# Kernel optimization log

Measured on AMD Instinct MI355X. Metric: run time of the kernel, lower is better.

## Reference

```python
import jax, jax.numpy as jnp
import numpy as np

B, S, D, H = 4, 1024, 1024, 16
HD = D // H  # head dim = 64


def setup_inputs() -> dict:
    key = jax.random.key(0)
    ks = jax.random.split(key, 12)
    inv = 1.0 / np.sqrt(D)
    inp = {
        "q": jax.random.normal(ks[0], (B, S, D), jnp.float32),
        "k": jax.random.normal(ks[1], (B, S, D), jnp.float32),
        "v": jax.random.normal(ks[2], (B, S, D), jnp.float32),
        # additive-style mask: 1 where attention is disallowed (causal)
        "mask": jnp.triu(jnp.ones((S, S), jnp.float32), k=1)[None, None, :, :],
        "Wq": jax.random.normal(ks[3], (D, D), jnp.float32) * inv,
        "bq": jnp.zeros((D,), jnp.float32),
        "Wk": jax.random.normal(ks[4], (D, D), jnp.float32) * inv,
        "bk": jnp.zeros((D,), jnp.float32),
        "Wv": jax.random.normal(ks[5], (D, D), jnp.float32) * inv,
        "bv": jnp.zeros((D,), jnp.float32),
        "Wo": jax.random.normal(ks[6], (D, D), jnp.float32) * inv,
        "bo": jnp.zeros((D,), jnp.float32),
    }
    return inp


def _split_heads(x):
    # [b, s, (h d)] -> [b, h, s, d]
    b, s, _ = x.shape
    return x.reshape(b, s, H, HD).transpose(0, 2, 1, 3)


def reference(q, k, v, mask, Wq, bq, Wk, bk, Wv, bv, Wo, bo):
    query = _split_heads(q @ Wq + bq)   # [b,h,s,d]
    key = _split_heads(k @ Wk + bk)
    value = _split_heads(v @ Wv + bv)

    scores = jnp.einsum("bhqd,bhkd->bhqk", query, key) / np.sqrt(HD)
    scores = scores + mask * (-1e12)
    attention_weights = jax.nn.softmax(scores, axis=-1)  # [b,h,s,s]
    attn = jnp.einsum("bhqk,bhkd->bhqd", attention_weights, value)

    # dropout is identity in eval mode
    attn = attn.transpose(0, 2, 1, 3).reshape(q.shape[0], q.shape[1], D)
    out = attn @ Wo + bo
    return out, attention_weights
```

## Files before the change

### kernel.cpp

```cpp
#include <hip/hip_runtime.h>
#include <hip/hip_bf16.h>

#define B_ 4
#define S_ 1024
#define D_ 1024
#define H_ 16
#define HD_ 64
#define M_ (B_*S_)
#define NT_ (S_/64)

typedef __attribute__((ext_vector_type(8))) short bf16x8;
typedef __attribute__((ext_vector_type(8))) unsigned short u16x8;
typedef __attribute__((ext_vector_type(4))) float f32x4;

typedef __attribute__((address_space(1))) const unsigned int g_uint;
typedef __attribute__((address_space(3))) unsigned int l_uint;

__device__ __forceinline__ unsigned short f2bf(float f) {
  unsigned int x = __builtin_bit_cast(unsigned int, f);
  unsigned int r = (x + 0x7fffu + ((x >> 16) & 1u)) >> 16;
  return (unsigned short)r;
}
__device__ __forceinline__ float bf2f(unsigned short u) {
  unsigned int x = ((unsigned int)u) << 16;
  return __builtin_bit_cast(float, x);
}
__device__ __forceinline__ void load_lds16(const ushort* g, ushort* l) {
  __builtin_amdgcn_global_load_lds((g_uint*)g, (l_uint*)l, 16, 0, 0);
}

__global__ void cvt3(const float* __restrict__ q, const float* __restrict__ k,
                     const float* __restrict__ v, ushort* __restrict__ qo,
                     ushort* __restrict__ ko, ushort* __restrict__ vo) {
  const float* s; ushort* d;
  switch (blockIdx.y) {
    case 0: s = q; d = qo; break;
    case 1: s = k; d = ko; break;
    default: s = v; d = vo; break;
  }
  int n4 = (M_ * D_) / 4;
  for (int i = blockIdx.x * blockDim.x + threadIdx.x; i < n4; i += gridDim.x * blockDim.x) {
    float4 x = reinterpret_cast<const float4*>(s)[i];
    ushort4 o;
    o.x = f2bf(x.x); o.y = f2bf(x.y); o.z = f2bf(x.z); o.w = f2bf(x.w);
    reinterpret_cast<ushort4*>(d)[i] = o;
  }
}

__global__ void tr4(const float* __restrict__ Wq, const float* __restrict__ Wk,
                    const float* __restrict__ Wv, const float* __restrict__ Wo,
                    ushort* __restrict__ q, ushort* __restrict__ k,
                    ushort* __restrict__ v, ushort* __restrict__ o) {
  const float* W; ushort* WT;
  switch (blockIdx.z) {
    case 0: W = Wq; WT = q; break;
    case 1: W = Wk; WT = k; break;
    case 2: W = Wv; WT = v; break;
    default: W = Wo; WT = o; break;
  }
  __shared__ float tile[32][33];
  int tx = threadIdx.x & 31, ty = threadIdx.x >> 5;
  int bx = blockIdx.x * 32, by = blockIdx.y * 32;
  for (int r = 0; r < 32; r += 8)
    tile[ty + r][tx] = W[(size_t)(by + ty + r) * D_ + bx + tx];
  __syncthreads();
  for (int r = 0; r < 32; r += 8)
    WT[(size_t)(bx + ty + r) * D_ + by + tx] = f2bf(tile[tx][ty + r]);
}

template <int BF16OUT>
__device__ __forceinline__ void gemm_body(const ushort* __restrict__ A,
                                          const ushort* __restrict__ Bt,
                                          const float* __restrict__ bias,
                                          void* __restrict__ Cp,
                                          int bm, int bn, int N, int K) {
  __shared__ ushort Al[128 * 64];
  __shared__ ushort Bl[128 * 64];
  const int tid = threadIdx.x;
  const int wave = tid >> 6, lane = tid & 63;
  const int r0 = lane & 15, kq = lane >> 4;
  const int wr = wave >> 1, wc = wave & 1;
  const int sl = lane >> 3;
  const int sc8 = ((lane & 7) ^ sl) * 8;
  f32x4 zero = {0.f, 0.f, 0.f, 0.f};
  f32x4 acc[4][4];
#pragma unroll
  for (int m = 0; m < 4; ++m)
#pragma unroll
    for (int n = 0; n < 4; ++n) acc[m][n] = zero;

  for (int kt = 0; kt < K; kt += 64) {
    __syncthreads();
#pragma unroll
    for (int i = 0; i < 4; ++i) {
      int c = wave * 4 + i;
      load_lds16(A  + (size_t)(bm + c * 8 + sl) * K + kt + sc8, &Al[c * 512]);
      load_lds16(Bt + (size_t)(bn + c * 8 + sl) * K + kt + sc8, &Bl[c * 512]);
    }
    __syncthreads();
#pragma unroll
    for (int kk = 0; kk < 2; ++kk) {
      bf16x8 a[4], b[4];
#pragma unroll
      for (int m = 0; m < 4; ++m)
        a[m] = *(const bf16x8*)&Al[(wr * 64 + m * 16 + r0) * 64 + (((kk * 4 + kq) ^ (r0 & 7)) * 8)];
#pragma unroll
      for (int n = 0; n < 4; ++n)
        b[n] = *(const bf16x8*)&Bl[(wc * 64 + n * 16 + r0) * 64 + (((kk * 4 + kq) ^ (r0 & 7)) * 8)];
#pragma unroll
      for (int m = 0; m < 4; ++m)
#pragma unroll
        for (int n = 0; n < 4; ++n)
          acc[m][n] = __builtin_amdgcn_mfma_f32_16x16x32_bf16(a[m], b[n], acc[m][n], 0, 0, 0);
    }
  }

#pragma unroll
  for (int m = 0; m < 4; ++m) {
#pragma unroll
    for (int n = 0; n < 4; ++n) {
      int col = bn + wc * 64 + n * 16 + r0;
      float bv = bias[col];
#pragma unroll
      for (int j = 0; j < 4; ++j) {
        int row = bm + wr * 64 + m * 16 + kq * 4 + j;
        float v = acc[m][n][j] + bv;
        if (BF16OUT) ((ushort*)Cp)[(size_t)row * N + col] = f2bf(v);
        else         ((float*)Cp)[(size_t)row * N + col] = v;
      }
    }
  }
}

__global__ __launch_bounds__(256) void gemm_qkv(const ushort* __restrict__ qa,
                                                const ushort* __restrict__ ka,
                                                const ushort* __restrict__ va,
                                                const ushort* __restrict__ WqT,
                                                const ushort* __restrict__ WkT,
                                                const ushort* __restrict__ WvT,
                                                const float* __restrict__ bq,
                                                const float* __restrict__ bk,
                                                const float* __restrict__ bv,
                                                ushort* __restrict__ Qo,
                                                ushort* __restrict__ Ko,
                                                ushort* __restrict__ Vo) {
  const ushort* A; const ushort* Bt; const float* bias; ushort* C;
  switch (blockIdx.z) {
    case 0: A = qa; Bt = WqT; bias = bq; C = Qo; break;
    case 1: A = ka; Bt = WkT; bias = bk; C = Ko; break;
    default: A = va; Bt = WvT; bias = bv; C = Vo; break;
  }
  gemm_body<1>(A, Bt, bias, C, blockIdx.x * 128, blockIdx.y * 128, D_, D_);
}

__global__ __launch_bounds__(256) void gemm_out(const ushort* __restrict__ A,
                                                const ushort* __restrict__ Bt,
                                                const float* __restrict__ bias,
                                                float* __restrict__ C) {
  gemm_body<0>(A, Bt, bias, C, blockIdx.x * 128, blockIdx.y * 128, D_, D_);
}

__global__ __launch_bounds__(256) void attn_fused(const ushort* __restrict__ Qb,
                                                  const ushort* __restrict__ Kb,
                                                  const ushort* __restrict__ Vb,
                                                  float* __restrict__ wout,
                                                  ushort* __restrict__ ctx) {
  const int id = blockIdx.x;
  const int h = (id & 7) | (((id >> 3) & 1) << 3);
  const int b = (id >> 4) & 3;
  const int px = id >> 6;
  const int tid = threadIdx.x, wave = tid >> 6, lane = tid & 63;
  const int r0 = lane & 15, kq = lane >> 4;
  const int sl = lane >> 3;
  const int sc8 = ((lane & 7) ^ sl) * 8;
  __shared__ ushort Kt[2][64 * 64];
  __shared__ ushort Vt[2][64 * 64];
  __shared__ ushort Wl[4][16 * 64];
  __shared__ float rs_lds[4][16];
  float* wbase = wout + (size_t)((b * H_ + h) * S_) * S_;
  const size_t bh_off = ((size_t)(b * S_)) * D_ + (size_t)h * 64;

  for (int pp = 0; pp < 2; ++pp) {
    const int qt = pp ? (NT_ - 1 - px) : px;
    __syncthreads();

    const ushort* Qg = Qb + bh_off + (size_t)(qt * 64 + wave * 16 + r0) * D_ + kq * 8;
    bf16x8 qa0 = *(const bf16x8*)Qg;
    bf16x8 qa1 = *(const bf16x8*)(Qg + 32);
    const int grow0 = qt * 64 + wave * 16 + kq * 4;

    auto stage_K = [&](int buf, int vb) {
      const ushort* Kg = Kb + bh_off + (size_t)(vb * 64) * D_;
#pragma unroll
      for (int i = 0; i < 2; ++i) {
        int c = wave * 2 + i;
        load_lds16(Kg + (size_t)(c * 8 + sl) * D_ + sc8, &Kt[buf][c * 512]);
      }
    };

    int cur = 0;
    stage_K(0, 0);
    float partial[4] = {0.f, 0.f, 0.f, 0.f};
    for (int vb = 0; vb <= qt; ++vb) {
      asm volatile("s_waitcnt vmcnt(0)" ::: "memory");
      __builtin_amdgcn_s_barrier();
      if (vb < qt) stage_K(cur ^ 1, vb + 1);
      const bool diag = (vb == qt);
#pragma unroll
      for (int jt = 0; jt < 4; ++jt) {
        int krow = jt * 16 + r0;
        bf16x8 kb0 = *(const bf16x8*)&Kt[cur][krow * 64 + ((kq ^ (r0 & 7)) * 8)];
        bf16x8 kb1 = *(const bf16x8*)&Kt[cur][krow * 64 + (((4 + kq) ^ (r0 & 7)) * 8)];
        f32x4 sc = {0.f, 0.f, 0.f, 0.f};
        sc = __builtin_amdgcn_mfma_f32_16x16x32_bf16(qa0, kb0, sc, 0, 0, 0);
        sc = __builtin_amdgcn_mfma_f32_16x16x32_bf16(qa1, kb1, sc, 0, 0, 0);
        int col = vb * 64 + krow;
#pragma unroll
        for (int j = 0; j < 4; ++j) {
          float e = (diag && col > grow0 + j) ? 0.f : __expf(sc[j] * 0.125f);
          partial[j] += e;
        }
      }
      cur ^= 1;
    }
    float rs[4];
#pragma unroll
    for (int j = 0; j < 4; ++j) {
      float s = partial[j];
#pragma unroll
      for (int off = 1; off < 16; off <<= 1) s += __shfl_xor(s, off, 64);
      rs[j] = 1.f / s;
    }
    if (r0 == 0) {
#pragma unroll
      for (int j = 0; j < 4; ++j) rs_lds[wave][kq * 4 + j] = rs[j];
    }

    f32x4 zero = {0.f, 0.f, 0.f, 0.f};
    f32x4 cacc[4];
#pragma unroll
    for (int nt = 0; nt < 4; ++nt) cacc[nt] = zero;

    __syncthreads();
    uint4 vr[2];
    auto vload = [&](int vb) {
      const ushort* Vg = Vb + bh_off + (size_t)(vb * 64) * D_;
      vr[0] = *(const uint4*)&Vg[(size_t)lane * D_ + (size_t)(wave * 2 + 0) * 8];
      vr[1] = *(const uint4*)&Vg[(size_t)lane * D_ + (size_t)(wave * 2 + 1) * 8];
    };
    auto vwrite = [&](int buf) {
#pragma unroll
      for (int it = 0; it < 2; ++it) {
        int seg = wave * 2 + it;
        ushort tmp[8];
        *(uint4*)tmp = vr[it];
#pragma unroll
        for (int e = 0; e < 8; ++e) Vt[buf][(seg * 8 + e) * 64 + (lane ^ (e << 3))] = tmp[e];
      }
    };
    cur = 0;
    stage_K(0, 0);
    vload(0);
    vwrite(0);
    for (int vb = 0; vb <= qt; ++vb) {
      asm volatile("s_waitcnt vmcnt(0) lgkmcnt(0)" ::: "memory");
      __builtin_amdgcn_s_barrier();
      if (vb < qt) { stage_K(cur ^ 1, vb + 1); vload(vb + 1); }
      const bool diag = (vb == qt);
#pragma unroll
      for (int jt = 0; jt < 4; ++jt) {
        int krow = jt * 16 + r0;
        bf16x8 kb0 = *(const bf16x8*)&Kt[cur][krow * 64 + ((kq ^ (r0 & 7)) * 8)];
        bf16x8 kb1 = *(const bf16x8*)&Kt[cur][krow * 64 + (((4 + kq) ^ (r0 & 7)) * 8)];
        f32x4 sc = {0.f, 0.f, 0.f, 0.f};
        sc = __builtin_amdgcn_mfma_f32_16x16x32_bf16(qa0, kb0, sc, 0, 0, 0);
        sc = __builtin_amdgcn_mfma_f32_16x16x32_bf16(qa1, kb1, sc, 0, 0, 0);
        int col = vb * 64 + krow;
#pragma unroll
        for (int j = 0; j < 4; ++j) {
          int rowW = kq * 4 + j;
          float e = (diag && col > grow0 + j) ? 0.f : __expf(sc[j] * 0.125f);
          Wl[wave][rowW * 64 + ((jt * 16 + r0) ^ ((rowW & 7) << 3))] = f2bf(e);
        }
      }
#pragma unroll
      for (int ks = 0; ks < 2; ++ks) {
        bf16x8 af = *(const bf16x8*)&Wl[wave][r0 * 64 + (((ks * 4 + kq) ^ (r0 & 7)) * 8)];
#pragma unroll
        for (int nt = 0; nt < 4; ++nt) {
          bf16x8 vf = *(const bf16x8*)&Vt[cur][(nt * 16 + r0) * 64 + (((ks * 4 + kq) ^ (r0 & 7)) * 8)];
          cacc[nt] = __builtin_amdgcn_mfma_f32_16x16x32_bf16(af, vf, cacc[nt], 0, 0, 0);
        }
      }
      {
        int row16 = lane >> 2, c4 = lane & 3;
        float scl = rs_lds[wave][row16];
        int slotA = (2 * c4) ^ (row16 & 7);
        int slotB = (2 * c4 + 1) ^ (row16 & 7);
        u16x8 w0 = *(const u16x8*)&Wl[wave][row16 * 64 + slotA * 8];
        u16x8 w1 = *(const u16x8*)&Wl[wave][row16 * 64 + slotB * 8];
        float* dst = &wbase[(size_t)(qt * 64 + wave * 16 + row16) * S_ + vb * 64 + c4 * 16];
        f32x4 o0 = {bf2f(w0[0]) * scl, bf2f(w0[1]) * scl, bf2f(w0[2]) * scl, bf2f(w0[3]) * scl};
        f32x4 o1 = {bf2f(w0[4]) * scl, bf2f(w0[5]) * scl, bf2f(w0[6]) * scl, bf2f(w0[7]) * scl};
        f32x4 o2 = {bf2f(w1[0]) * scl, bf2f(w1[1]) * scl, bf2f(w1[2]) * scl, bf2f(w1[3]) * scl};
        f32x4 o3 = {bf2f(w1[4]) * scl, bf2f(w1[5]) * scl, bf2f(w1[6]) * scl, bf2f(w1[7]) * scl};
        *(f32x4*)&dst[0]  = o0;
        *(f32x4*)&dst[4]  = o1;
        *(f32x4*)&dst[8]  = o2;
        *(f32x4*)&dst[12] = o3;
      }
      if (vb < qt) vwrite(cur ^ 1);
      cur ^= 1;
    }

    {
      int col0 = (qt + 1) * 64;
      int nf4 = (S_ - col0) >> 2;
      int row = tid >> 2, c = tid & 3;
      f32x4 z4 = {0.f, 0.f, 0.f, 0.f};
      float* rp = &wbase[(size_t)(qt * 64 + row) * S_];
      for (int i = c; i < nf4; i += 4) *(f32x4*)&rp[col0 + i * 4] = z4;
    }

    {
      ushort* cg = ctx + ((size_t)(b * S_ + qt * 64 + wave * 16 + kq * 4)) * D_ + h * 64;
#pragma unroll
      for (int nt = 0; nt < 4; ++nt)
#pragma unroll
        for (int j = 0; j < 4; ++j)
          cg[(size_t)j * D_ + nt * 16 + r0] = f2bf(cacc[nt][j] * rs[j]);
    }
  }
}

extern "C" void kernel_launch(void* const* d_in, const int* in_sizes, int n_in,
                              void* d_out, int out_size, void* d_ws, size_t ws_size,
                              hipStream_t stream) {
  const float* q    = (const float*)d_in[0];
  const float* k    = (const float*)d_in[1];
  const float* v    = (const float*)d_in[2];
  const float* Wq   = (const float*)d_in[4];
  const float* bq   = (const float*)d_in[5];
  const float* Wk   = (const float*)d_in[6];
  const float* bk   = (const float*)d_in[7];
  const float* Wv   = (const float*)d_in[8];
  const float* bv   = (const float*)d_in[9];
  const float* Wo   = (const float*)d_in[10];
  const float* bo   = (const float*)d_in[11];

  char* ws = (char*)d_ws;
  const size_t MB = 1024 * 1024;
  ushort* q_bf   = (ushort*)(ws + 0 * MB);
  ushort* k_bf   = (ushort*)(ws + 8 * MB);
  ushort* v_bf   = (ushort*)(ws + 16 * MB);
  ushort* WqT    = (ushort*)(ws + 24 * MB);
  ushort* WkT    = (ushort*)(ws + 26 * MB);
  ushort* WvT    = (ushort*)(ws + 28 * MB);
  ushort* WoT    = (ushort*)(ws + 30 * MB);
  ushort* Q_bf   = (ushort*)(ws + 32 * MB);
  ushort* K_bf   = (ushort*)(ws + 40 * MB);
  ushort* V_bf   = (ushort*)(ws + 48 * MB);
  ushort* ctx_bf = (ushort*)(ws + 56 * MB);

  float* out  = (float*)d_out;
  float* wout = out + (size_t)M_ * D_;

  cvt3<<<dim3(2048, 3), 256, 0, stream>>>(q, k, v, q_bf, k_bf, v_bf);
  tr4<<<dim3(32, 32, 4), 256, 0, stream>>>(Wq, Wk, Wv, Wo, WqT, WkT, WvT, WoT);
  gemm_qkv<<<dim3(M_ / 128, D_ / 128, 3), 256, 0, stream>>>(
      q_bf, k_bf, v_bf, WqT, WkT, WvT, bq, bk, bv, Q_bf, K_bf, V_bf);
  attn_fused<<<dim3(512), 256, 0, stream>>>(Q_bf, K_bf, V_bf, wout, ctx_bf);
  gemm_out<<<dim3(M_ / 128, D_ / 128), 256, 0, stream>>>(ctx_bf, WoT, bo, out);
}
```

Before: 175.7 us.

## Split fused attention into row-sum pass and PV/weights pass kernels

The single attention kernel, which handled two paired query tiles per block in two sequential passes, becomes two kernels. The first computes softmax row reciprocals into a workspace buffer that reuses the q_bf region. The second recomputes scores, writes normalized weights and computes the context. Both launch 1024 blocks, one query tile each, heaviest tiles first, and K is now read straight from global memory instead of being staged in LDS. This aims for more parallelism and lower LDS use, at the cost of an extra launch, a global round trip for the sums, and uncoalesced-ish K loads that rely on cache.

New measurement: 215.6 us. 1.23x slower.

```diff
diff --git a/kernel.cpp b/kernel.cpp
--- a/kernel.cpp
+++ b/kernel.cpp
@@ -160,176 +160,174 @@
   gemm_body<0>(A, Bt, bias, C, blockIdx.x * 128, blockIdx.y * 128, D_, D_);
 }
 
-__global__ __launch_bounds__(256) void attn_fused(const ushort* __restrict__ Qb,
-                                                  const ushort* __restrict__ Kb,
-                                                  const ushort* __restrict__ Vb,
-                                                  float* __restrict__ wout,
-                                                  ushort* __restrict__ ctx) {
+__global__ __launch_bounds__(256) void attn_sums(const ushort* __restrict__ Qb,
+                                                 const ushort* __restrict__ Kb,
+                                                 float* __restrict__ rsum) {
   const int id = blockIdx.x;
-  const int h = (id & 7) | (((id >> 3) & 1) << 3);
-  const int b = (id >> 4) & 3;
-  const int px = id >> 6;
+  const int bh = id & 63;
+  const int b = bh >> 4, h = bh & 15;
+  const int qt = NT_ - 1 - (id >> 6);
   const int tid = threadIdx.x, wave = tid >> 6, lane = tid & 63;
   const int r0 = lane & 15, kq = lane >> 4;
-  const int sl = lane >> 3;
-  const int sc8 = ((lane & 7) ^ sl) * 8;
-  __shared__ ushort Kt[2][64 * 64];
+  const size_t bh_off = ((size_t)(b * S_)) * D_ + (size_t)h * 64;
+
+  const ushort* Qg = Qb + bh_off + (size_t)(qt * 64 + wave * 16 + r0) * D_ + kq * 8;
+  bf16x8 qa0 = *(const bf16x8*)Qg;
+  bf16x8 qa1 = *(const bf16x8*)(Qg + 32);
+  const int grow0 = qt * 64 + wave * 16 + kq * 4;
+
+  float partial[4] = {0.f, 0.f, 0.f, 0.f};
+  const ushort* Kg0 = Kb + bh_off;
+  for (int vb = 0; vb <= qt; ++vb) {
+    const ushort* Kg = Kg0 + (size_t)(vb * 64) * D_;
+    const bool diag = (vb == qt);
+#pragma unroll
+    for (int jt = 0; jt < 4; ++jt) {
+      int krow = jt * 16 + r0;
+      bf16x8 kb0 = *(const bf16x8*)&Kg[(size_t)krow * D_ + kq * 8];
+      bf16x8 kb1 = *(const bf16x8*)&Kg[(size_t)krow * D_ + 32 + kq * 8];
+      f32x4 sc = {0.f, 0.f, 0.f, 0.f};
+      sc = __builtin_amdgcn_mfma_f32_16x16x32_bf16(qa0, kb0, sc, 0, 0, 0);
+      sc = __builtin_amdgcn_mfma_f32_16x16x32_bf16(qa1, kb1, sc, 0, 0, 0);
+      int col = vb * 64 + krow;
+#pragma unroll
+      for (int j = 0; j < 4; ++j) {
+        float e = (diag && col > grow0 + j) ? 0.f : __expf(sc[j] * 0.125f);
+        partial[j] += e;
+      }
+    }
+  }
+  f32x4 rs4;
+#pragma unroll
+  for (int j = 0; j < 4; ++j) {
+    float s = partial[j];
+#pragma unroll
+    for (int off = 1; off < 16; off <<= 1) s += __shfl_xor(s, off, 64);
+    rs4[j] = 1.f / s;
+  }
+  if (r0 == 0)
+    *(f32x4*)&rsum[(size_t)bh * S_ + qt * 64 + wave * 16 + kq * 4] = rs4;
+}
+
+__global__ __launch_bounds__(256) void attn_pv(const ushort* __restrict__ Qb,
+                                               const ushort* __restrict__ Kb,
+                                               const ushort* __restrict__ Vb,
+                                               const float* __restrict__ rsum,
+                                               float* __restrict__ wout,
+                                               ushort* __restrict__ ctx) {
+  const int id = blockIdx.x;
+  const int bh = id & 63;
+  const int b = bh >> 4, h = bh & 15;
+  const int qt = NT_ - 1 - (id >> 6);
+  const int tid = threadIdx.x, wave = tid >> 6, lane = tid & 63;
+  const int r0 = lane & 15, kq = lane >> 4;
   __shared__ ushort Vt[2][64 * 64];
   __shared__ ushort Wl[4][16 * 64];
-  __shared__ float rs_lds[4][16];
-  float* wbase = wout + (size_t)((b * H_ + h) * S_) * S_;
   const size_t bh_off = ((size_t)(b * S_)) * D_ + (size_t)h * 64;
-
-  for (int pp = 0; pp < 2; ++pp) {
-    const int qt = pp ? (NT_ - 1 - px) : px;
-    __syncthreads();
-
-    const ushort* Qg = Qb + bh_off + (size_t)(qt * 64 + wave * 16 + r0) * D_ + kq * 8;
-    bf16x8 qa0 = *(const bf16x8*)Qg;
-    bf16x8 qa1 = *(const bf16x8*)(Qg + 32);
-    const int grow0 = qt * 64 + wave * 16 + kq * 4;
-
-    auto stage_K = [&](int buf, int vb) {
-      const ushort* Kg = Kb + bh_off + (size_t)(vb * 64) * D_;
-#pragma unroll
-      for (int i = 0; i < 2; ++i) {
-        int c = wave * 2 + i;
-        load_lds16(Kg + (size_t)(c * 8 + sl) * D_ + sc8, &Kt[buf][c * 512]);
+  float* wbase = wout + (size_t)bh * S_ * S_;
+
+  const ushort* Qg = Qb + bh_off + (size_t)(qt * 64 + wave * 16 + r0) * D_ + kq * 8;
+  bf16x8 qa0 = *(const bf16x8*)Qg;
+  bf16x8 qa1 = *(const bf16x8*)(Qg + 32);
+  const int grow0 = qt * 64 + wave * 16 + kq * 4;
+
+  const float* rsrow = rsum + (size_t)bh * S_ + qt * 64 + wave * 16;
+  f32x4 rs4 = *(const f32x4*)&rsrow[kq * 4];
+  float sclw = rsrow[lane >> 2];
+
+  uint4 vr[2];
+  auto vload = [&](int vb) {
+    const ushort* Vg = Vb + bh_off + (size_t)(vb * 64) * D_;
+    vr[0] = *(const uint4*)&Vg[(size_t)lane * D_ + (size_t)(wave * 2 + 0) * 8];
+    vr[1] = *(const uint4*)&Vg[(size_t)lane * D_ + (size_t)(wave * 2 + 1) * 8];
+  };
+  auto vwrite = [&](int buf) {
+#pragma unroll
+    for (int it = 0; it < 2; ++it) {
+      int seg = wave * 2 + it;
+      ushort tmp[8];
+      *(uint4*)tmp = vr[it];
+#pragma unroll
+      for (int e = 0; e < 8; ++e) Vt[buf][(seg * 8 + e) * 64 + (lane ^ (e << 3))] = tmp[e];
+    }
+  };
+
+  f32x4 zero = {0.f, 0.f, 0.f, 0.f};
+  f32x4 cacc[4];
+#pragma unroll
+  for (int nt = 0; nt < 4; ++nt) cacc[nt] = zero;
+
+  int cur = 0;
+  vload(0);
+  vwrite(0);
+  const ushort* Kg0 = Kb + bh_off;
+  for (int vb = 0; vb <= qt; ++vb) {
+    asm volatile("s_waitcnt lgkmcnt(0)" ::: "memory");
+    __builtin_amdgcn_s_barrier();
+    if (vb < qt) vload(vb + 1);
+    const bool diag = (vb == qt);
+    const ushort* Kg = Kg0 + (size_t)(vb * 64) * D_;
+#pragma unroll
+    for (int jt = 0; jt < 4; ++jt) {
+      int krow = jt * 16 + r0;
+      bf16x8 kb0 = *(const bf16x8*)&Kg[(size_t)krow * D_ + kq * 8];
+      bf16x8 kb1 = *(const bf16x8*)&Kg[(size_t)krow * D_ + 32 + kq * 8];
+      f32x4 sc = {0.f, 0.f, 0.f, 0.f};
+      sc = __builtin_amdgcn_mfma_f32_16x16x32_bf16(qa0, kb0, sc, 0, 0, 0);
+      sc = __builtin_amdgcn_mfma_f32_16x16x32_bf16(qa1, kb1, sc, 0, 0, 0);
+      int col = vb * 64 + krow;
+#pragma unroll
+      for (int j = 0; j < 4; ++j) {
+        int rowW = kq * 4 + j;
+        float e = (diag && col > grow0 + j) ? 0.f : __expf(sc[j] * 0.125f);
+        Wl[wave][rowW * 64 + ((jt * 16 + r0) ^ ((rowW & 7) << 3))] = f2bf(e);
       }
-    };
-
-    int cur = 0;
-    stage_K(0, 0);
-    float partial[4] = {0.f, 0.f, 0.f, 0.f};
-    for (int vb = 0; vb <= qt; ++vb) {
-      asm volatile("s_waitcnt vmcnt(0)" ::: "memory");
-      __builtin_amdgcn_s_barrier();
-      if (vb < qt) stage_K(cur ^ 1, vb + 1);
-      const bool diag = (vb == qt);
-#pragma unroll
-      for (int jt = 0; jt < 4; ++jt) {
-        int krow = jt * 16 + r0;
-        bf16x8 kb0 = *(const bf16x8*)&Kt[cur][krow * 64 + ((kq ^ (r0 & 7)) * 8)];
-        bf16x8 kb1 = *(const bf16x8*)&Kt[cur][krow * 64 + (((4 + kq) ^ (r0 & 7)) * 8)];
-        f32x4 sc = {0.f, 0.f, 0.f, 0.f};
-        sc = __builtin_amdgcn_mfma_f32_16x16x32_bf16(qa0, kb0, sc, 0, 0, 0);
-        sc = __builtin_amdgcn_mfma_f32_16x16x32_bf16(qa1, kb1, sc, 0, 0, 0);
-        int col = vb * 64 + krow;
-#pragma unroll
-        for (int j = 0; j < 4; ++j) {
-          float e = (diag && col > grow0 + j) ? 0.f : __expf(sc[j] * 0.125f);
-          partial[j] += e;
-        }
+    }
+#pragma unroll
+    for (int ks = 0; ks < 2; ++ks) {
+      bf16x8 af = *(const bf16x8*)&Wl[wave][r0 * 64 + (((ks * 4 + kq) ^ (r0 & 7)) * 8)];
+#pragma unroll
+      for (int nt = 0; nt < 4; ++nt) {
+        bf16x8 vf = *(const bf16x8*)&Vt[cur][(nt * 16 + r0) * 64 + (((ks * 4 + kq) ^ (r0 & 7)) * 8)];
+        cacc[nt] = __builtin_amdgcn_mfma_f32_16x16x32_bf16(af, vf, cacc[nt], 0, 0, 0);
       }
-      cur ^= 1;
-    }
-    float rs[4];
-#pragma unroll
-    for (int j = 0; j < 4; ++j) {
-      float s = partial[j];
-#pragma unroll
-      for (int off = 1; off < 16; off <<= 1) s += __shfl_xor(s, off, 64);
-      rs[j] = 1.f / s;
-    }
-    if (r0 == 0) {
-#pragma unroll
-      for (int j = 0; j < 4; ++j) rs_lds[wave][kq * 4 + j] = rs[j];
-    }
-
-    f32x4 zero = {0.f, 0.f, 0.f, 0.f};
-    f32x4 cacc[4];
-#pragma unroll
-    for (int nt = 0; nt < 4; ++nt) cacc[nt] = zero;
-
-    __syncthreads();
-    uint4 vr[2];
-    auto vload = [&](int vb) {
-      const ushort* Vg = Vb + bh_off + (size_t)(vb * 64) * D_;
-      vr[0] = *(const uint4*)&Vg[(size_t)lane * D_ + (size_t)(wave * 2 + 0) * 8];
-      vr[1] = *(const uint4*)&Vg[(size_t)lane * D_ + (size_t)(wave * 2 + 1) * 8];
-    };
-    auto vwrite = [&](int buf) {
-#pragma unroll
-      for (int it = 0; it < 2; ++it) {
-        int seg = wave * 2 + it;
-        ushort tmp[8];
-        *(uint4*)tmp = vr[it];
-#pragma unroll
-        for (int e = 0; e < 8; ++e) Vt[buf][(seg * 8 + e) * 64 + (lane ^ (e << 3))] = tmp[e];
-      }
-    };
-    cur = 0;
-    stage_K(0, 0);
-    vload(0);
-    vwrite(0);
-    for (int vb = 0; vb <= qt; ++vb) {
-      asm volatile("s_waitcnt vmcnt(0) lgkmcnt(0)" ::: "memory");
-      __builtin_amdgcn_s_barrier();
-      if (vb < qt) { stage_K(cur ^ 1, vb + 1); vload(vb + 1); }
-      const bool diag = (vb == qt);
-#pragma unroll
-      for (int jt = 0; jt < 4; ++jt) {
-        int krow = jt * 16 + r0;
-        bf16x8 kb0 = *(const bf16x8*)&Kt[cur][krow * 64 + ((kq ^ (r0 & 7)) * 8)];
-        bf16x8 kb1 = *(const bf16x8*)&Kt[cur][krow * 64 + (((4 + kq) ^ (r0 & 7)) * 8)];
-        f32x4 sc = {0.f, 0.f, 0.f, 0.f};
-        sc = __builtin_amdgcn_mfma_f32_16x16x32_bf16(qa0, kb0, sc, 0, 0, 0);
-        sc = __builtin_amdgcn_mfma_f32_16x16x32_bf16(qa1, kb1, sc, 0, 0, 0);
-        int col = vb * 64 + krow;
-#pragma unroll
-        for (int j = 0; j < 4; ++j) {
-          int rowW = kq * 4 + j;
-          float e = (diag && col > grow0 + j) ? 0.f : __expf(sc[j] * 0.125f);
-          Wl[wave][rowW * 64 + ((jt * 16 + r0) ^ ((rowW & 7) << 3))] = f2bf(e);
-        }
-      }
-#pragma unroll
-      for (int ks = 0; ks < 2; ++ks) {
-        bf16x8 af = *(const bf16x8*)&Wl[wave][r0 * 64 + (((ks * 4 + kq) ^ (r0 & 7)) * 8)];
-#pragma unroll
-        for (int nt = 0; nt < 4; ++nt) {
-          bf16x8 vf = *(const bf16x8*)&Vt[cur][(nt * 16 + r0) * 64 + (((ks * 4 + kq) ^ (r0 & 7)) * 8)];
-          cacc[nt] = __builtin_amdgcn_mfma_f32_16x16x32_bf16(af, vf, cacc[nt], 0, 0, 0);
-        }
-      }
-      {
-        int row16 = lane >> 2, c4 = lane & 3;
-        float scl = rs_lds[wave][row16];
-        int slotA = (2 * c4) ^ (row16 & 7);
-        int slotB = (2 * c4 + 1) ^ (row16 & 7);
-        u16x8 w0 = *(const u16x8*)&Wl[wave][row16 * 64 + slotA * 8];
-        u16x8 w1 = *(const u16x8*)&Wl[wave][row16 * 64 + slotB * 8];
-        float* dst = &wbase[(size_t)(qt * 64 + wave * 16 + row16) * S_ + vb * 64 + c4 * 16];
-        f32x4 o0 = {bf2f(w0[0]) * scl, bf2f(w0[1]) * scl, bf2f(w0[2]) * scl, bf2f(w0[3]) * scl};
-        f32x4 o1 = {bf2f(w0[4]) * scl, bf2f(w0[5]) * scl, bf2f(w0[6]) * scl, bf2f(w0[7]) * scl};
-        f32x4 o2 = {bf2f(w1[0]) * scl, bf2f(w1[1]) * scl, bf2f(w1[2]) * scl, bf2f(w1[3]) * scl};
-        f32x4 o3 = {bf2f(w1[4]) * scl, bf2f(w1[5]) * scl, bf2f(w1[6]) * scl, bf2f(w1[7]) * scl};
-        *(f32x4*)&dst[0]  = o0;
-        *(f32x4*)&dst[4]  = o1;
-        *(f32x4*)&dst[8]  = o2;
-        *(f32x4*)&dst[12] = o3;
-      }
-      if (vb < qt) vwrite(cur ^ 1);
-      cur ^= 1;
-    }
-
+    }
     {
-      int col0 = (qt + 1) * 64;
-      int nf4 = (S_ - col0) >> 2;
-      int row = tid >> 2, c = tid & 3;
-      f32x4 z4 = {0.f, 0.f, 0.f, 0.f};
-      float* rp = &wbase[(size_t)(qt * 64 + row) * S_];
-      for (int i = c; i < nf4; i += 4) *(f32x4*)&rp[col0 + i * 4] = z4;
-    }
-
-    {
-      ushort* cg = ctx + ((size_t)(b * S_ + qt * 64 + wave * 16 + kq * 4)) * D_ + h * 64;
-#pragma unroll
-      for (int nt = 0; nt < 4; ++nt)
-#pragma unroll
-        for (int j = 0; j < 4; ++j)
-          cg[(size_t)j * D_ + nt * 16 + r0] = f2bf(cacc[nt][j] * rs[j]);
-    }
+      int row16 = lane >> 2, c4 = lane & 3;
+      int slotA = (2 * c4) ^ (row16 & 7);
+      int slotB = (2 * c4 + 1) ^ (row16 & 7);
+      u16x8 w0 = *(const u16x8*)&Wl[wave][row16 * 64 + slotA * 8];
+      u16x8 w1 = *(const u16x8*)&Wl[wave][row16 * 64 + slotB * 8];
+      float* dst = &wbase[(size_t)(qt * 64 + wave * 16 + row16) * S_ + vb * 64 + c4 * 16];
+      f32x4 o0 = {bf2f(w0[0]) * sclw, bf2f(w0[1]) * sclw, bf2f(w0[2]) * sclw, bf2f(w0[3]) * sclw};
+      f32x4 o1 = {bf2f(w0[4]) * sclw, bf2f(w0[5]) * sclw, bf2f(w0[6]) * sclw, bf2f(w0[7]) * sclw};
+      f32x4 o2 = {bf2f(w1[0]) * sclw, bf2f(w1[1]) * sclw, bf2f(w1[2]) * sclw, bf2f(w1[3]) * sclw};
+      f32x4 o3 = {bf2f(w1[4]) * sclw, bf2f(w1[5]) * sclw, bf2f(w1[6]) * sclw, bf2f(w1[7]) * sclw};
+      *(f32x4*)&dst[0]  = o0;
+      *(f32x4*)&dst[4]  = o1;
+      *(f32x4*)&dst[8]  = o2;
+      *(f32x4*)&dst[12] = o3;
+    }
+    if (vb < qt) vwrite(cur ^ 1);
+    cur ^= 1;
+  }
+
+  {
+    int col0 = (qt + 1) * 64;
+    int nf4 = (S_ - col0) >> 2;
+    int row = tid >> 2, c = tid & 3;
+    f32x4 z4 = {0.f, 0.f, 0.f, 0.f};
+    float* rp = &wbase[(size_t)(qt * 64 + row) * S_];
+    for (int i = c; i < nf4; i += 4) *(f32x4*)&rp[col0 + i * 4] = z4;
+  }
+
+  {
+    ushort* cg = ctx + ((size_t)(b * S_ + qt * 64 + wave * 16 + kq * 4)) * D_ + h * 64;
+#pragma unroll
+    for (int nt = 0; nt < 4; ++nt)
+#pragma unroll
+      for (int j = 0; j < 4; ++j)
+        cg[(size_t)j * D_ + nt * 16 + r0] = f2bf(cacc[nt][j] * rs4[j]);
   }
 }
 
@@ -361,6 +359,7 @@
   ushort* K_bf   = (ushort*)(ws + 40 * MB);
   ushort* V_bf   = (ushort*)(ws + 48 * MB);
   ushort* ctx_bf = (ushort*)(ws + 56 * MB);
+  float*  rsum   = (float*)(ws + 0 * MB);
 
   float* out  = (float*)d_out;
   float* wout = out + (size_t)M_ * D_;
@@ -369,6 +368,7 @@
   tr4<<<dim3(32, 32, 4), 256, 0, stream>>>(Wq, Wk, Wv, Wo, WqT, WkT, WvT, WoT);
   gemm_qkv<<<dim3(M_ / 128, D_ / 128, 3), 256, 0, stream>>>(
       q_bf, k_bf, v_bf, WqT, WkT, WvT, bq, bk, bv, Q_bf, K_bf, V_bf);
-  attn_fused<<<dim3(512), 256, 0, stream>>>(Q_bf, K_bf, V_bf, wout, ctx_bf);
+  attn_sums<<<dim3(1024), 256, 0, stream>>>(Q_bf, K_bf, rsum);
+  attn_pv<<<dim3(1024), 256, 0, stream>>>(Q_bf, K_bf, V_bf, rsum, wout, ctx_bf);
   gemm_out<<<dim3(M_ / 128, D_ / 128), 256, 0, stream>>>(ctx_bf, WoT, bo, out);
 }
```
